# Kernel tuning notes

Measured on AMD Instinct MI355X. Metric: run time of the kernel, lower is better.

## Reference

```python
import jax, jax.numpy as jnp
from jax import lax
import numpy as np

N_SAMPLES = 65536
SPB = 512            # samples_per_block
H, W = 32, 32        # room_dim
N_BLOCKS = N_SAMPLES // SPB   # 128
ENV = 16             # impulse_envelope_size
NCOEF = SPB // 2 + 1 # 257
MIC = (16, 16)


def setup_inputs() -> dict:
    key = jax.random.key(0)
    k1, k2, k3, k4 = jax.random.split(key, 4)
    x = jax.random.normal(k1, (1, 1, N_SAMPLES), dtype=jnp.float32)
    transfer_functions = jax.random.uniform(k2, (N_BLOCKS, H, W, NCOEF), dtype=jnp.float32)
    impulses = jax.random.uniform(k3, (N_BLOCKS, H, W, ENV), dtype=jnp.float32) * 0.001
    noise = jax.random.uniform(k4, (N_BLOCKS, H, W, SPB), dtype=jnp.float32, minval=-1.0, maxval=1.0)
    return {"x": x, "transfer_functions": transfer_functions,
            "impulses": impulses, "noise": noise}


def _box3_mean(sf):
    # sf: (H, W, SPB). 3x3 box mean with reflect padding (kernel=ones, mean over 3x3).
    p = jnp.pad(sf, ((1, 1), (1, 1), (0, 0)), mode='reflect')
    acc = p[0:H, 0:W]
    for i in range(3):
        for j in range(3):
            if i == 0 and j == 0:
                continue
            acc = acc + p[i:i + H, j:j + W]
    return acc / 9.0


def reference(x, transfer_functions, impulses, noise):
    # x is accepted (signature fidelity) but unused, as in the original forward.
    def step(sound_field, inputs):
        imp, tf, nz = inputs  # (H,W,ENV), (H,W,NCOEF), (H,W,SPB)
        # F.interpolate(mode='linear') == half-pixel linear resize along last axis
        env = jax.image.resize(imp, (H, W, SPB), method='linear')
        env = jnp.clip(env, 0.0, 1.0) * nz
        resonance = jnp.clip(tf, 0.0, 1.0)
        spec = jnp.fft.rfft(env, norm='ortho')            # (H,W,NCOEF) complex64
        filtered = jnp.fft.irfft(resonance * spec, n=SPB, norm='ortho')
        sound_field = sound_field + filtered
        mic_sig = sound_field[MIC[0], MIC[1]]             # (SPB,)
        sound_field = _box3_mean(sound_field)
        return sound_field, mic_sig

    sf0 = jnp.zeros((H, W, SPB), dtype=jnp.float32)
    _, mic = lax.scan(step, sf0, (impulses, transfer_functions, noise))
    final = mic.reshape(1, 1, -1)[..., :N_SAMPLES]
    return final
```

## Files before the change

kernel.cpp:

```cpp
#include <hip/hip_runtime.h>
#include <hip/hip_fp16.h>

#define NB   128
#define SPB_ 512
#define NPOS 131072
#define NBIN 256
#define PI_F 3.14159265358979323846f
#define R2_F 0.70710678118654752f

template<int CTRL>
static __device__ __forceinline__ float fdpp(float x) {
    union { float f; int i; } a, r;
    a.f = x;
    r.i = __builtin_amdgcn_update_dpp(a.i, a.i, CTRL, 0xF, 0xF, false);
    return r.f;
}

typedef unsigned uv2_t __attribute__((ext_vector_type(2)));

static __device__ __forceinline__ void swap16pair(float x, float& lo, float& hi) {
#if __has_builtin(__builtin_amdgcn_permlane16_swap)
    union { float f; unsigned u; } a; a.f = x;
    uv2_t r = __builtin_amdgcn_permlane16_swap(a.u, a.u, false, false);
    union { unsigned u; float f; } o0, o1; o0.u = r[0]; o1.u = r[1];
    lo = o0.f; hi = o1.f;
#else
    float other = __shfl_xor(x, 16, 64);
    bool hb = (threadIdx.x & 16) != 0;
    lo = hb ? other : x; hi = hb ? x : other;
#endif
}

static __device__ __forceinline__ void swap32pair(float x, float& lo, float& hi) {
#if __has_builtin(__builtin_amdgcn_permlane32_swap)
    union { float f; unsigned u; } a; a.f = x;
    uv2_t r = __builtin_amdgcn_permlane32_swap(a.u, a.u, false, false);
    union { unsigned u; float f; } o0, o1; o0.u = r[0]; o1.u = r[1];
    lo = o0.f; hi = o1.f;
#else
    float other = __shfl_xor(x, 32, 64);
    bool hb = (threadIdx.x & 32) != 0;
    lo = hb ? other : x; hi = hb ? x : other;
#endif
}

template<int T>
static __device__ __forceinline__ void cross_stage(
    float er[4][4], float ei[4][4], float c0, float s0,
    const float* wjcR, const float* wjsR, int lane)
{
    const int lm = 1 << T;
    #pragma unroll
    for (int j = 0; j < 4; ++j) {
        float c, s;
        if (j == 0) { c = c0; s = s0; }
        else {
            c = c0 * wjcR[j - 1] - s0 * wjsR[j - 1];
            s = c0 * wjsR[j - 1] + s0 * wjcR[j - 1];
        }
        #pragma unroll
        for (int p = 0; p < 4; ++p) {
            float lr, li, hr, hi_;
            if constexpr (T == 0) {
                lr  = fdpp<0xA0>(er[p][j]); hr  = fdpp<0xF5>(er[p][j]);
                li  = fdpp<0xA0>(ei[p][j]); hi_ = fdpp<0xF5>(ei[p][j]);
            } else if constexpr (T == 1) {
                lr  = fdpp<0x44>(er[p][j]); hr  = fdpp<0xEE>(er[p][j]);
                li  = fdpp<0x44>(ei[p][j]); hi_ = fdpp<0xEE>(ei[p][j]);
            } else if constexpr (T == 2 || T == 3) {
                float orr = __shfl_xor(er[p][j], lm, 64);
                float oii = __shfl_xor(ei[p][j], lm, 64);
                const bool hb = (lane & lm) != 0;
                lr = hb ? orr : er[p][j]; hr  = hb ? er[p][j] : orr;
                li = hb ? oii : ei[p][j]; hi_ = hb ? ei[p][j] : oii;
            } else if constexpr (T == 4) {
                swap16pair(er[p][j], lr, hr);
                swap16pair(ei[p][j], li, hi_);
            } else {
                swap32pair(er[p][j], lr, hr);
                swap32pair(ei[p][j], li, hi_);
            }
            er[p][j] = fmaf(c, hr,  fmaf(-s, hi_, lr));
            ei[p][j] = fmaf(c, hi_, fmaf( s, hr,  li));
        }
    }
}

__global__ __launch_bounds__(256) void k1_fft(
    const float* __restrict__ tf,
    const float* __restrict__ imp,
    const float* __restrict__ nz,
    __half2* __restrict__ Hbuf)
{
    __shared__ float   ldsImp[256];
    __shared__ __half2 stg[16][260];

    const int tid  = threadIdx.x;
    const int wv   = tid >> 6;
    const int lane = tid & 63;
    const int pos0 = blockIdx.x << 4;

    ldsImp[tid] = imp[(size_t)pos0 * 16 + tid];

    const int B = __brev((unsigned)lane) >> 26;
    const int offj[4] = {0, 128, 64, 192};

    float bc[6], bs[6];
    #pragma unroll
    for (int t = 0; t < 6; ++t) {
        const int lm = 1 << t;
        float ang = -PI_F * (float)(lane & (lm - 1)) / (float)lm;
        __sincosf(ang, &bs[t], &bc[t]);
        if (lane & lm) { bc[t] = -bc[t]; bs[t] = -bs[t]; }
    }
    float uc, us;
    __sincosf(-PI_F * (1.0f / 64.0f) * (float)lane, &us, &uc);

    float fru[4][2]; int j0u[4][2];
    #pragma unroll
    for (int j = 0; j < 4; ++j)
        #pragma unroll
        for (int u = 0; u < 2; ++u) {
            int   t = 2 * (B + offj[j]) + u;
            float p = ((float)t - 15.5f) * (1.0f / 32.0f);
            p = fminf(fmaxf(p, 0.0f), 15.0f);
            int j0 = (int)p; j0 = j0 > 14 ? 14 : j0;
            j0u[j][u] = j0; fru[j][u] = p - (float)j0;
        }

    const float wjc[6][3] = {
        {R2_F, 0.0f, -R2_F},
        {0.92387953f, 0.70710678f, 0.38268343f},
        {0.98078528f, 0.92387953f, 0.83146961f},
        {0.99518473f, 0.98078528f, 0.95694034f},
        {0.99879546f, 0.99518473f, 0.98917651f},
        {0.99969882f, 0.99879546f, 0.99729046f}};
    const float wjs[6][3] = {
        {-R2_F, -1.0f, -R2_F},
        {-0.38268343f, -0.70710678f, -0.92387953f},
        {-0.19509032f, -0.38268343f, -0.55557023f},
        {-0.09801714f, -0.19509032f, -0.29028468f},
        {-0.04906767f, -0.09801714f, -0.14673047f},
        {-0.02454123f, -0.04906767f, -0.07356456f}};
    const float ujc[3] = {0.99992470f, 0.99969882f, 0.99932238f};
    const float ujs[3] = {-0.01227154f, -0.02454123f, -0.03680722f};

    __syncthreads();

    const int rA = wv << 2;

    float2 q[4][4];
    #pragma unroll
    for (int p = 0; p < 4; ++p) {
        const float2* nzp = (const float2*)(nz + (size_t)(pos0 + rA + p) * SPB_);
        #pragma unroll
        for (int r = 0; r < 4; ++r) q[p][r] = nzp[lane + (r << 6)];
    }

    const int rb2[4] = {0, 2, 1, 3};
    float er[4][4], ei[4][4];
    #pragma unroll
    for (int p = 0; p < 4; ++p) {
        const int base = (rA + p) << 4;
        #pragma unroll
        for (int j = 0; j < 4; ++j) {
            float gx = __shfl(q[p][rb2[j]].x, B, 64);
            float gy = __shfl(q[p][rb2[j]].y, B, 64);
            float a0 = ldsImp[base + j0u[j][0]];
            float b0 = ldsImp[base + j0u[j][0] + 1];
            float a1 = ldsImp[base + j0u[j][1]];
            float b1 = ldsImp[base + j0u[j][1] + 1];
            er[p][j] = fmaf(fru[j][0], b0 - a0, a0) * gx;
            ei[p][j] = fmaf(fru[j][1], b1 - a1, a1) * gy;
        }
    }

    #pragma unroll
    for (int p = 0; p < 4; ++p) {
        float ar, ai, br, bi;
        ar = er[p][0]; ai = ei[p][0]; br = er[p][1]; bi = ei[p][1];
        er[p][0] = ar + br; ei[p][0] = ai + bi;
        er[p][1] = ar - br; ei[p][1] = ai - bi;
        ar = er[p][2]; ai = ei[p][2]; br = er[p][3]; bi = ei[p][3];
        er[p][2] = ar + br; ei[p][2] = ai + bi;
        er[p][3] = ar - br; ei[p][3] = ai - bi;
        ar = er[p][0]; ai = ei[p][0]; br = er[p][2]; bi = ei[p][2];
        er[p][0] = ar + br; ei[p][0] = ai + bi;
        er[p][2] = ar - br; ei[p][2] = ai - bi;
        ar = er[p][1]; ai = ei[p][1]; br = er[p][3]; bi = ei[p][3];
        er[p][1] = ar + bi; ei[p][1] = ai - br;
        er[p][3] = ar - bi; ei[p][3] = ai + br;
    }

    float tfv[4][4], tf256[4];
    #pragma unroll
    for (int p = 0; p < 4; ++p) {
        const float* tfp = tf + (size_t)(pos0 + rA + p) * 257;
        #pragma unroll
        for (int j = 0; j < 4; ++j) tfv[p][j] = tfp[4 * lane + j];
        tf256[p] = tfp[256];
    }

    cross_stage<0>(er, ei, bc[0], bs[0], wjc[0], wjs[0], lane);
    cross_stage<1>(er, ei, bc[1], bs[1], wjc[1], wjs[1], lane);
    cross_stage<2>(er, ei, bc[2], bs[2], wjc[2], wjs[2], lane);
    cross_stage<3>(er, ei, bc[3], bs[3], wjc[3], wjs[3], lane);
    cross_stage<4>(er, ei, bc[4], bs[4], wjc[4], wjs[4], lane);
    cross_stage<5>(er, ei, bc[5], bs[5], wjc[5], wjs[5], lane);

    const int pl = (64 - lane) & 63;
    #pragma unroll
    for (int p = 0; p < 4; ++p) {
        const int row = rA + p;
        float pr[4], pi[4];
        pr[0] = __shfl(er[p][0], pl, 64);  pi[0] = __shfl(ei[p][0], pl, 64);
        pr[1] = __shfl_xor(er[p][3], 63, 64); pi[1] = __shfl_xor(ei[p][3], 63, 64);
        pr[2] = __shfl_xor(er[p][2], 63, 64); pi[2] = __shfl_xor(ei[p][2], 63, 64);
        pr[3] = __shfl_xor(er[p][1], 63, 64); pi[3] = __shfl_xor(ei[p][1], 63, 64);

        __half2 hv[4];
        #pragma unroll
        for (int j = 0; j < 4; ++j) {
            float E2r = er[p][j] + pr[j], E2i = ei[p][j] - pi[j];
            float O2r = ei[p][j] + pi[j], O2i = pr[j] - er[p][j];
            float cv, sv;
            if (j == 0) { cv = uc; sv = us; }
            else {
                cv = uc * ujc[j - 1] - us * ujs[j - 1];
                sv = uc * ujs[j - 1] + us * ujc[j - 1];
            }
            float Xr = E2r + cv * O2r - sv * O2i;
            float Xi = E2i + cv * O2i + sv * O2r;
            float rk = 0.5f * tfv[p][j];
            hv[j] = __floats2half2_rn(rk * Xr, rk * Xi);
            if (j == 0 && lane == 0) {
                hv[0] = __floats2half2_rn(0.5f * tfv[p][0] * (E2r + O2r),
                                          0.5f * tf256[p]  * (E2r - O2r));
            }
        }
        union { float4 v; __half2 h[4]; } u4;
        u4.h[0] = hv[0]; u4.h[1] = hv[1]; u4.h[2] = hv[2]; u4.h[3] = hv[3];
        *(float4*)&stg[row][4 * lane] = u4.v;
    }

    __syncthreads();
    {
        const int rr = tid & 15, kb = tid >> 4;
        const size_t pbase = (size_t)pos0 + rr;
        #pragma unroll
        for (int i = 0; i < 16; ++i) {
            int k = kb + (i << 4);
            Hbuf[(size_t)k * NPOS + pbase] = stg[rr][k];
        }
    }
}

__global__ __launch_bounds__(1024) void k2_scan(
    const __half2* __restrict__ Hbuf,
    float2* __restrict__ Mbuf)
{
    __shared__ float2 sfb[2][32][33];
    const int k   = blockIdx.x;
    const int tid = threadIdx.x;
    const int h   = tid >> 5, w = tid & 31;
    const int hm = (h == 0) ? 1 : h - 1, hp = (h == 31) ? 30 : h + 1;
    const int wm = (w == 0) ? 1 : w - 1, wp = (w == 31) ? 30 : w + 1;

    const __half2* Hp = Hbuf + (size_t)k * NPOS + tid;
    __half2 c0 = Hp[0];
    __half2 c1 = Hp[1024];
    float fr = 0.0f, fi = 0.0f;

    for (int b = 0; b < NB; ++b) {
        float2 hv = __half22float2(c0);
        c0 = c1;
        if (b + 2 < NB) c1 = Hp[(size_t)(b + 2) << 10];
        fr += hv.x; fi += hv.y;
        if (tid == 528) Mbuf[b * NBIN + k] = make_float2(fr, fi);
        sfb[b & 1][h][w] = make_float2(fr, fi);
        __syncthreads();
        float sr = 0.0f, si = 0.0f; float2 v;
        v = sfb[b & 1][hm][wm]; sr += v.x; si += v.y;
        v = sfb[b & 1][hm][w ]; sr += v.x; si += v.y;
        v = sfb[b & 1][hm][wp]; sr += v.x; si += v.y;
        v = sfb[b & 1][h ][wm]; sr += v.x; si += v.y;
        v = sfb[b & 1][h ][w ]; sr += v.x; si += v.y;
        v = sfb[b & 1][h ][wp]; sr += v.x; si += v.y;
        v = sfb[b & 1][hp][wm]; sr += v.x; si += v.y;
        v = sfb[b & 1][hp][w ]; sr += v.x; si += v.y;
        v = sfb[b & 1][hp][wp]; sr += v.x; si += v.y;
        fr = sr * (1.0f / 9.0f); fi = si * (1.0f / 9.0f);
    }
}

__global__ __launch_bounds__(512) void k3_idft(
    const float2* __restrict__ Mbuf,
    float* __restrict__ out)
{
    __shared__ float2 lm[256];
    const int b = blockIdx.x;
    const int t = threadIdx.x;
    if (t < 256) lm[t] = Mbuf[b * NBIN + t];
    __syncthreads();
    float acc = 0.0f;
    #pragma unroll 4
    for (int k = 1; k < 256; ++k) {
        int   ph  = (k * t) & 511;
        float ang = (float)ph * (PI_F / 256.0f);
        float sv, cv; __sincosf(ang, &sv, &cv);
        float2 m = lm[k];
        acc += m.x * cv - m.y * sv;
    }
    float m0 = lm[0].x, m256 = lm[0].y;
    float r  = m0 + ((t & 1) ? -m256 : m256) + 2.0f * acc;
    out[(b << 9) + t] = r * (1.0f / 512.0f);
}

extern "C" void kernel_launch(void* const* d_in, const int* in_sizes, int n_in,
                              void* d_out, int out_size, void* d_ws, size_t ws_size,
                              hipStream_t stream)
{
    const float* tf  = (const float*)d_in[1];
    const float* imp = (const float*)d_in[2];
    const float* nz  = (const float*)d_in[3];
    float* out = (float*)d_out;

    const size_t hbytes = (size_t)NBIN * NPOS * sizeof(__half2);
    const size_t mbytes = (size_t)NB * NBIN * sizeof(float2);
    if (ws_size < hbytes + mbytes) {
        (void)hipMemsetAsync(d_out, 0xFF, (size_t)out_size * sizeof(float), stream);
        return;
    }
    __half2* Hbuf = (__half2*)d_ws;
    float2*  Mbuf = (float2*)((char*)d_ws + hbytes);

    k1_fft<<<NPOS / 16, 256, 0, stream>>>(tf, imp, nz, Hbuf);
    k2_scan<<<NBIN, 1024, 0, stream>>>(Hbuf, Mbuf);
    k3_idft<<<NB, 512, 0, stream>>>(Mbuf, out);
}
```

Before: 195.9 us.

## Process eight FFT rows per wave in k1 with 128-thread blocks

Halves the k1 block size to two waves, each handling eight rows instead of four, so twiddle setup and per-wave constants are amortized over more FFTs. Noise is now gathered directly in bit-reversed order from global memory instead of through wave shuffles. The stage-3 exchange uses a DPP row operation instead of a shuffle, and the transfer-function loads move after the butterflies. The cost is higher register pressure, possibly lower occupancy, and uncoalesced noise loads.

```diff
diff --git a/kernel.cpp b/kernel.cpp
--- a/kernel.cpp
+++ b/kernel.cpp
@@ -45,11 +45,10 @@
 }
 
 template<int T>
-static __device__ __forceinline__ void cross_stage(
-    float er[4][4], float ei[4][4], float c0, float s0,
+static __device__ __forceinline__ void cross_stage8(
+    float er[8][4], float ei[8][4], float c0, float s0,
     const float* wjcR, const float* wjsR, int lane)
 {
-    const int lm = 1 << T;
     #pragma unroll
     for (int j = 0; j < 4; ++j) {
         float c, s;
@@ -59,7 +58,7 @@
             s = c0 * wjsR[j - 1] + s0 * wjcR[j - 1];
         }
         #pragma unroll
-        for (int p = 0; p < 4; ++p) {
+        for (int p = 0; p < 8; ++p) {
             float lr, li, hr, hi_;
             if constexpr (T == 0) {
                 lr  = fdpp<0xA0>(er[p][j]); hr  = fdpp<0xF5>(er[p][j]);
@@ -67,10 +66,16 @@
             } else if constexpr (T == 1) {
                 lr  = fdpp<0x44>(er[p][j]); hr  = fdpp<0xEE>(er[p][j]);
                 li  = fdpp<0x44>(ei[p][j]); hi_ = fdpp<0xEE>(ei[p][j]);
-            } else if constexpr (T == 2 || T == 3) {
-                float orr = __shfl_xor(er[p][j], lm, 64);
-                float oii = __shfl_xor(ei[p][j], lm, 64);
-                const bool hb = (lane & lm) != 0;
+            } else if constexpr (T == 2) {
+                float orr = __shfl_xor(er[p][j], 4, 64);
+                float oii = __shfl_xor(ei[p][j], 4, 64);
+                const bool hb = (lane & 4) != 0;
+                lr = hb ? orr : er[p][j]; hr  = hb ? er[p][j] : orr;
+                li = hb ? oii : ei[p][j]; hi_ = hb ? ei[p][j] : oii;
+            } else if constexpr (T == 3) {
+                float orr = fdpp<0x128>(er[p][j]);
+                float oii = fdpp<0x128>(ei[p][j]);
+                const bool hb = (lane & 8) != 0;
                 lr = hb ? orr : er[p][j]; hr  = hb ? er[p][j] : orr;
                 li = hb ? oii : ei[p][j]; hi_ = hb ? ei[p][j] : oii;
             } else if constexpr (T == 4) {
@@ -86,7 +91,7 @@
     }
 }
 
-__global__ __launch_bounds__(256) void k1_fft(
+__global__ __launch_bounds__(128) void k1_fft(
     const float* __restrict__ tf,
     const float* __restrict__ imp,
     const float* __restrict__ nz,
@@ -100,7 +105,7 @@
     const int lane = tid & 63;
     const int pos0 = blockIdx.x << 4;
 
-    ldsImp[tid] = imp[(size_t)pos0 * 16 + tid];
+    ((float2*)ldsImp)[tid] = ((const float2*)(imp + (size_t)pos0 * 16))[tid];
 
     const int B = __brev((unsigned)lane) >> 26;
     const int offj[4] = {0, 128, 64, 192};
@@ -147,36 +152,27 @@
 
     __syncthreads();
 
-    const int rA = wv << 2;
-
-    float2 q[4][4];
-    #pragma unroll
-    for (int p = 0; p < 4; ++p) {
+    const int rA = wv << 3;
+
+    float er[8][4], ei[8][4];
+    #pragma unroll
+    for (int p = 0; p < 8; ++p) {
         const float2* nzp = (const float2*)(nz + (size_t)(pos0 + rA + p) * SPB_);
-        #pragma unroll
-        for (int r = 0; r < 4; ++r) q[p][r] = nzp[lane + (r << 6)];
-    }
-
-    const int rb2[4] = {0, 2, 1, 3};
-    float er[4][4], ei[4][4];
-    #pragma unroll
-    for (int p = 0; p < 4; ++p) {
         const int base = (rA + p) << 4;
         #pragma unroll
         for (int j = 0; j < 4; ++j) {
-            float gx = __shfl(q[p][rb2[j]].x, B, 64);
-            float gy = __shfl(q[p][rb2[j]].y, B, 64);
+            float2 g = nzp[B + offj[j]];
             float a0 = ldsImp[base + j0u[j][0]];
             float b0 = ldsImp[base + j0u[j][0] + 1];
             float a1 = ldsImp[base + j0u[j][1]];
             float b1 = ldsImp[base + j0u[j][1] + 1];
-            er[p][j] = fmaf(fru[j][0], b0 - a0, a0) * gx;
-            ei[p][j] = fmaf(fru[j][1], b1 - a1, a1) * gy;
-        }
-    }
-
-    #pragma unroll
-    for (int p = 0; p < 4; ++p) {
+            er[p][j] = fmaf(fru[j][0], b0 - a0, a0) * g.x;
+            ei[p][j] = fmaf(fru[j][1], b1 - a1, a1) * g.y;
+        }
+    }
+
+    #pragma unroll
+    for (int p = 0; p < 8; ++p) {
         float ar, ai, br, bi;
         ar = er[p][0]; ai = ei[p][0]; br = er[p][1]; bi = ei[p][1];
         er[p][0] = ar + br; ei[p][0] = ai + bi;
@@ -192,25 +188,25 @@
         er[p][3] = ar - bi; ei[p][3] = ai + br;
     }
 
-    float tfv[4][4], tf256[4];
-    #pragma unroll
-    for (int p = 0; p < 4; ++p) {
+    cross_stage8<0>(er, ei, bc[0], bs[0], wjc[0], wjs[0], lane);
+    cross_stage8<1>(er, ei, bc[1], bs[1], wjc[1], wjs[1], lane);
+    cross_stage8<2>(er, ei, bc[2], bs[2], wjc[2], wjs[2], lane);
+    cross_stage8<3>(er, ei, bc[3], bs[3], wjc[3], wjs[3], lane);
+    cross_stage8<4>(er, ei, bc[4], bs[4], wjc[4], wjs[4], lane);
+    cross_stage8<5>(er, ei, bc[5], bs[5], wjc[5], wjs[5], lane);
+
+    float tfv[8][4], tf256[8];
+    #pragma unroll
+    for (int p = 0; p < 8; ++p) {
         const float* tfp = tf + (size_t)(pos0 + rA + p) * 257;
         #pragma unroll
         for (int j = 0; j < 4; ++j) tfv[p][j] = tfp[4 * lane + j];
         tf256[p] = tfp[256];
     }
 
-    cross_stage<0>(er, ei, bc[0], bs[0], wjc[0], wjs[0], lane);
-    cross_stage<1>(er, ei, bc[1], bs[1], wjc[1], wjs[1], lane);
-    cross_stage<2>(er, ei, bc[2], bs[2], wjc[2], wjs[2], lane);
-    cross_stage<3>(er, ei, bc[3], bs[3], wjc[3], wjs[3], lane);
-    cross_stage<4>(er, ei, bc[4], bs[4], wjc[4], wjs[4], lane);
-    cross_stage<5>(er, ei, bc[5], bs[5], wjc[5], wjs[5], lane);
-
     const int pl = (64 - lane) & 63;
     #pragma unroll
-    for (int p = 0; p < 4; ++p) {
+    for (int p = 0; p < 8; ++p) {
         const int row = rA + p;
         float pr[4], pi[4];
         pr[0] = __shfl(er[p][0], pl, 64);  pi[0] = __shfl(ei[p][0], pl, 64);
@@ -248,8 +244,8 @@
         const int rr = tid & 15, kb = tid >> 4;
         const size_t pbase = (size_t)pos0 + rr;
         #pragma unroll
-        for (int i = 0; i < 16; ++i) {
-            int k = kb + (i << 4);
+        for (int i = 0; i < 32; ++i) {
+            int k = kb + (i << 3);
             Hbuf[(size_t)k * NPOS + pbase] = stg[rr][k];
         }
     }
@@ -334,7 +330,7 @@
     __half2* Hbuf = (__half2*)d_ws;
     float2*  Mbuf = (float2*)((char*)d_ws + hbytes);
 
-    k1_fft<<<NPOS / 16, 256, 0, stream>>>(tf, imp, nz, Hbuf);
+    k1_fft<<<NPOS / 16, 128, 0, stream>>>(tf, imp, nz, Hbuf);
     k2_scan<<<NBIN, 1024, 0, stream>>>(Hbuf, Mbuf);
     k3_idft<<<NB, 512, 0, stream>>>(Mbuf, out);
 }
```

Result: slower. 214.4 us (+9.4%).
